# Kernel tuning notes

Measured on AMD Instinct MI355X. Metric: run time of the kernel, lower is better.

## Reference

```python
import jax, jax.numpy as jnp
import numpy as np

B, D, H, S, REP, OUT = 4096, 256, 256, 3, 10, 44


def setup_inputs():
    key = jax.random.key(0)
    ks = jax.random.split(key, 30)
    def rn(k, shape, scale=1.0):
        return jax.random.normal(k, shape, dtype=jnp.float32) * scale
    w = 0.05
    return {
        "x": rn(ks[0], (B, D)),
        "hidden0": rn(ks[1], (S, B, H)),
        "current0": rn(ks[2], (S, B, H)),
        "Wi_f": rn(ks[3], (S, H, D), w), "bi_f": rn(ks[4], (S, H), w),
        "Wi_i": rn(ks[5], (S, H, D), w), "bi_i": rn(ks[6], (S, H), w),
        "Wi_o": rn(ks[7], (S, H, D), w), "bi_o": rn(ks[8], (S, H), w),
        "Wi_c": rn(ks[9], (S, H, D), w), "bi_c": rn(ks[10], (S, H), w),
        "Wi_g": rn(ks[11], (S, S, D), w), "bi_g": rn(ks[12], (S, S), w),
        "Wh_f": rn(ks[13], (S, H, H), w), "bh_f": rn(ks[14], (S, H), w),
        "Wh_i": rn(ks[15], (S, H, H), w), "bh_i": rn(ks[16], (S, H), w),
        "Wh_o": rn(ks[17], (S, H, H), w), "bh_o": rn(ks[18], (S, H), w),
        "Wh_g": rn(ks[19], (S, S, S * H), w), "bh_g": rn(ks[20], (S, S), w),
        "Wh_c": rn(ks[21], (S, S * H, S * H), w), "bh_c": rn(ks[22], (S, S * H), w),
        "W_last": rn(ks[23], (OUT, (REP - 1) * H), w), "b_last": rn(ks[24], (OUT,), w),
    }


def _lin(x, W, b):
    return x @ W.T + b


def _gflstm(x, hidden0, current0, Wi_f, bi_f, Wi_i, bi_i, Wi_o, bi_o, Wi_c, bi_c,
            Wi_g, bi_g, Wh_f, bh_f, Wh_i, bh_i, Wh_o, bh_o, Wh_g, bh_g,
            Wh_c, bh_c, W_last, b_last):
    S_, B_, H_ = hidden0.shape
    rep = W_last.shape[1] // H_ + 1  # (rep_time-1)*H in-features of last layer
    h_prev, c_prev = hidden0, current0
    last_layer_hs = []
    for t in range(rep):  # fixed small trip-count, sequential recurrence
        # torch.cat(hidden[t], 1): layer-major concat -> [B, S*H]
        h_cat = jnp.transpose(h_prev, (1, 0, 2)).reshape(B_, S_ * H_)
        input_h = x
        h_list, c_list = [], []
        for l in range(S_):
            f = jax.nn.sigmoid(_lin(input_h, Wi_f[l], bi_f[l]) + _lin(h_prev[l], Wh_f[l], bh_f[l]))
            i = jax.nn.sigmoid(_lin(input_h, Wi_i[l], bi_i[l]) + _lin(h_prev[l], Wh_i[l], bh_i[l]))
            g = jax.nn.sigmoid(_lin(input_h, Wi_g[l], bi_g[l]) + _lin(h_cat, Wh_g[l], bh_g[l]))  # [B, S]
            aux = _lin(h_cat, Wh_c[l], bh_c[l]).reshape(B_, S_, H_)
            aux = (aux * g[:, :, None]).sum(axis=1)  # gated cross-layer weighted sum -> [B, H]
            c_t = jnp.tanh(_lin(input_h, Wi_c[l], bi_c[l]) + aux)
            c = f * c_prev[l] + i * c_t
            o = jax.nn.sigmoid(_lin(input_h, Wi_o[l], bi_o[l]) + _lin(h_prev[l], Wh_o[l], bh_o[l]))
            h = o * c
            input_h = h
            h_list.append(h)
            c_list.append(c)
        h_prev = jnp.stack(h_list)
        c_prev = jnp.stack(c_list)
        if t < rep - 1:  # output uses hidden[1..rep-1][-1]
            last_layer_hs.append(h_list[-1])
    feat = jnp.concatenate(last_layer_hs, axis=1)  # [B, (rep-1)*H]
    return jax.nn.sigmoid(_lin(feat, W_last, b_last))


def reference(x, hidden0, current0, Wi_f, bi_f, Wi_i, bi_i, Wi_o, bi_o, Wi_c, bi_c,
              Wi_g, bi_g, Wh_f, bh_f, Wh_i, bh_i, Wh_o, bh_o, Wh_g, bh_g,
              Wh_c, bh_c, W_last, b_last):
    return _gflstm(x, hidden0, current0, Wi_f, bi_f, Wi_i, bi_i, Wi_o, bi_o, Wi_c, bi_c,
                   Wi_g, bi_g, Wh_f, bh_f, Wh_i, bh_i, Wh_o, bh_o, Wh_g, bh_g,
                   Wh_c, bh_c, W_last, b_last)
```

## Files before the change

### kernel.cpp

```cpp
#include <hip/hip_runtime.h>
#include <hip/hip_bf16.h>

typedef __hip_bfloat16 bf16;
typedef __attribute__((ext_vector_type(8))) short frag8;
typedef __attribute__((ext_vector_type(4))) float f32x4;

#define BM 128
#define BN 128
#define BK 64
#define SK 72

__device__ __forceinline__ float sigm(float x) { return 1.f / (1.f + __expf(-x)); }

__device__ __forceinline__ void lds_load16(const bf16* g, short* l) {
    __builtin_amdgcn_global_load_lds(
        (const __attribute__((address_space(1))) void*)g,
        (__attribute__((address_space(3))) void*)l, 16, 0, 0);
}

__global__ __launch_bounds__(256, 2)
void gemm_bt(const bf16* __restrict__ A, int lda, long long sAz,
             const bf16* __restrict__ W, int ldw, long long sWz,
             void* __restrict__ Cv, int ldc, long long sCz, int K,
             int outmode, const float* __restrict__ bias, int nbound,
             const bf16* __restrict__ Wg, float* __restrict__ gout)
{
    __shared__ short As[BM * SK];
    __shared__ short Bs[BN * SK];
    __shared__ short Bg[16 * SK];
    const int z = blockIdx.z;
    A += (size_t)z * sAz;
    W += (size_t)z * sWz;
    const int m0 = blockIdx.y * BM;
    const int n0 = blockIdx.x * BN;
    const int tid  = threadIdx.x;
    const int lane = tid & 63;
    const int wave = tid >> 6;
    const int wm = (wave >> 1) * 64;
    const int wn = (wave & 1) * 64;
    const int q   = lane >> 4;
    const int r16 = lane & 15;
    const bool do_g = (Wg != nullptr) && (blockIdx.x == 0);

    f32x4 acc[4][4] = {};
    f32x4 accg[4] = {};

    const int trow = tid >> 3;
    const int tcol = (tid & 7) * 8;

    for (int k0 = 0; k0 < K; k0 += BK) {
        __syncthreads();
        #pragma unroll
        for (int p = 0; p < 4; ++p) {
            int rr = p * 32 + trow;
            *(uint4*)&As[rr * SK + tcol] =
                *(const uint4*)(A + (size_t)(m0 + rr) * lda + k0 + tcol);
            *(uint4*)&Bs[rr * SK + tcol] =
                *(const uint4*)(W + (size_t)(n0 + rr) * ldw + k0 + tcol);
        }
        if (do_g && tid < 128)
            *(uint4*)&Bg[(tid >> 3) * SK + tcol] =
                *(const uint4*)(Wg + (size_t)(tid >> 3) * 256 + k0 + tcol);
        __syncthreads();
        #pragma unroll
        for (int kk = 0; kk < 2; ++kk) {
            const int ko = kk * 32 + q * 8;
            frag8 af[4], bfr[4];
            #pragma unroll
            for (int i = 0; i < 4; ++i)
                af[i] = *(const frag8*)&As[(wm + i * 16 + r16) * SK + ko];
            #pragma unroll
            for (int j = 0; j < 4; ++j)
                bfr[j] = *(const frag8*)&Bs[(wn + j * 16 + r16) * SK + ko];
            #pragma unroll
            for (int i = 0; i < 4; ++i)
                #pragma unroll
                for (int j = 0; j < 4; ++j)
                    acc[i][j] = __builtin_amdgcn_mfma_f32_16x16x32_bf16(
                        af[i], bfr[j], acc[i][j], 0, 0, 0);
            if (do_g) {
                frag8 bg = *(const frag8*)&Bg[r16 * SK + ko];
                #pragma unroll
                for (int i = 0; i < 4; ++i)
                    accg[i] = __builtin_amdgcn_mfma_f32_16x16x32_bf16(
                        af[i], bg, accg[i], 0, 0, 0);
            }
        }
    }

    if (outmode == 0) {
        float* C = (float*)Cv + (size_t)z * sCz;
        #pragma unroll
        for (int i = 0; i < 4; ++i)
            #pragma unroll
            for (int rr = 0; rr < 4; ++rr) {
                int row = m0 + wm + i * 16 + q * 4 + rr;
                float* crow = C + (size_t)row * ldc + n0 + wn + r16;
                #pragma unroll
                for (int j = 0; j < 4; ++j) crow[j * 16] = acc[i][j][rr];
            }
    } else if (outmode == 1) {
        bf16* C = (bf16*)Cv + (size_t)z * sCz;
        #pragma unroll
        for (int i = 0; i < 4; ++i)
            #pragma unroll
            for (int rr = 0; rr < 4; ++rr) {
                int row = m0 + wm + i * 16 + q * 4 + rr;
                bf16* crow = C + (size_t)row * ldc + n0 + wn + r16;
                #pragma unroll
                for (int j = 0; j < 4; ++j) crow[j * 16] = __float2bfloat16(acc[i][j][rr]);
            }
    } else if (outmode == 2) {
        float* C = (float*)Cv + (size_t)z * sCz;
        #pragma unroll
        for (int i = 0; i < 4; ++i)
            #pragma unroll
            for (int rr = 0; rr < 4; ++rr) {
                int row = m0 + wm + i * 16 + q * 4 + rr;
                #pragma unroll
                for (int j = 0; j < 4; ++j) {
                    int col = n0 + wn + j * 16 + r16;
                    if (col < nbound)
                        C[(size_t)row * ldc + col] = sigm(acc[i][j][rr] + bias[col]);
                }
            }
    } else {
        float* C = (float*)Cv + (size_t)z * sCz;
        #pragma unroll
        for (int i = 0; i < 4; ++i)
            #pragma unroll
            for (int rr = 0; rr < 4; ++rr) {
                int row = m0 + wm + i * 16 + q * 4 + rr;
                #pragma unroll
                for (int j = 0; j < 4; ++j) {
                    int col = n0 + wn + j * 16 + r16;
                    if (col < nbound)
                        C[(size_t)row * ldc + col] = acc[i][j][rr];
                }
            }
    }
    if (do_g && wn == 0 && r16 < 3) {
        #pragma unroll
        for (int i = 0; i < 4; ++i)
            #pragma unroll
            for (int rr = 0; rr < 4; ++rr) {
                int row = m0 + wm + i * 16 + q * 4 + rr;
                gout[(size_t)row * 3 + r16] = accg[i][rr];
            }
    }
}

__global__ __launch_bounds__(256, 3)
void gemm_hidden(const bf16* __restrict__ hprev,
                 const bf16* __restrict__ WhFIO,
                 const bf16* __restrict__ WhCb,
                 const bf16* __restrict__ WgH,
                 const float* __restrict__ big, const float* __restrict__ bhg,
                 bf16* __restrict__ hgb,
                 bf16* __restrict__ auxb,
                 float* __restrict__ gh)
{
    __shared__ __align__(16) short As[BM * 64];
    __shared__ __align__(16) short Bs[BN * 64];
    __shared__ __align__(16) short Bg[16 * 64];

    const int zi = blockIdx.x % 6;
    const int xt = blockIdx.x / 6;
    const bool isaux = zi >= 3;
    const int l = isaux ? zi - 3 : zi;
    const bf16* A = hprev + (isaux ? 0 : l * 256);
    const int K = isaux ? 768 : 256;
    const bf16* W = isaux ? (WhCb + (size_t)l * 768 * 768) : (WhFIO + (size_t)l * 768 * 256);
    const int ldw = isaux ? 768 : 256;
    bf16* C = (isaux ? auxb : hgb) + (size_t)l * 4096 * 768;
    const bool do_g = isaux && (xt == 0);

    const int m0 = blockIdx.y * BM;
    const int n0 = xt * BN;
    const int tid  = threadIdx.x;
    const int lane = tid & 63;
    const int wave = tid >> 6;
    const int wm = (wave >> 1) * 64;
    const int wn = (wave & 1) * 64;
    const int q   = lane >> 4;
    const int r16 = lane & 15;

    f32x4 acc[4][4] = {};
    f32x4 accg[4] = {};

    const int srow = lane >> 3;
    const int scolsw = ((lane & 7) ^ srow) * 8;
    const bf16* WgL = WgH + (size_t)l * 16 * 768;

    for (int k0 = 0; k0 < K; k0 += BK) {
        __syncthreads();
        #pragma unroll
        for (int p = 0; p < 4; ++p) {
            int rbase = (wave * 4 + p) * 8;
            lds_load16(A + (size_t)(m0 + rbase + srow) * 768 + k0 + scolsw, &As[rbase * 64]);
            lds_load16(W + (size_t)(n0 + rbase + srow) * ldw + k0 + scolsw, &Bs[rbase * 64]);
        }
        if (do_g && wave < 2)
            lds_load16(WgL + (size_t)(wave * 8 + srow) * 768 + k0 + scolsw, &Bg[wave * 8 * 64]);
        __syncthreads();
        #pragma unroll
        for (int kk = 0; kk < 2; ++kk) {
            const int c = kk * 4 + q;
            frag8 af[4], bfr[4];
            #pragma unroll
            for (int i = 0; i < 4; ++i) {
                int R = wm + i * 16 + r16;
                af[i] = *(const frag8*)&As[R * 64 + ((c ^ (R & 7)) << 3)];
            }
            #pragma unroll
            for (int j = 0; j < 4; ++j) {
                int R = wn + j * 16 + r16;
                bfr[j] = *(const frag8*)&Bs[R * 64 + ((c ^ (R & 7)) << 3)];
            }
            #pragma unroll
            for (int i = 0; i < 4; ++i)
                #pragma unroll
                for (int j = 0; j < 4; ++j)
                    acc[i][j] = __builtin_amdgcn_mfma_f32_16x16x32_bf16(
                        af[i], bfr[j], acc[i][j], 0, 0, 0);
            if (do_g) {
                frag8 bg = *(const frag8*)&Bg[r16 * 64 + ((c ^ (r16 & 7)) << 3)];
                #pragma unroll
                for (int i = 0; i < 4; ++i)
                    accg[i] = __builtin_amdgcn_mfma_f32_16x16x32_bf16(
                        af[i], bg, accg[i], 0, 0, 0);
            }
        }
    }

    #pragma unroll
    for (int i = 0; i < 4; ++i)
        #pragma unroll
        for (int rr = 0; rr < 4; ++rr) {
            int row = m0 + wm + i * 16 + q * 4 + rr;
            bf16* crow = C + (size_t)row * 768 + n0 + wn + r16;
            #pragma unroll
            for (int j = 0; j < 4; ++j) crow[j * 16] = __float2bfloat16(acc[i][j][rr]);
        }
    if (do_g && wn == 0 && r16 < 3) {
        float bsum = big[l * 3 + r16] + bhg[l * 3 + r16];
        #pragma unroll
        for (int i = 0; i < 4; ++i)
            #pragma unroll
            for (int rr = 0; rr < 4; ++rr) {
                int row = m0 + wm + i * 16 + q * 4 + rr;
                gh[(size_t)row * 9 + l * 3 + r16] = accg[i][rr] + bsum;
            }
    }
}

#define GM 32
struct Stage { short As[GM * 64]; short Bs[BN * 64]; short Bg[16 * 64]; };
union SMemU { Stage s; float ct[GM * 128]; };

__global__ __launch_bounds__(256, 2)
void gemm_gates(const bf16* __restrict__ A, int lda,
                const bf16* __restrict__ Wi, const bf16* __restrict__ Wg,
                const bf16* __restrict__ hg_l,
                const bf16* __restrict__ aux_l,
                const float* __restrict__ ghc_l,
                const float* __restrict__ cprev,
                const float* __restrict__ bif, const float* __restrict__ bhf,
                const float* __restrict__ bii, const float* __restrict__ bhi,
                const float* __restrict__ bio, const float* __restrict__ bho,
                const float* __restrict__ bic, const float* __restrict__ bhc,
                bf16*  __restrict__ hnew,
                float* __restrict__ cnew,
                bf16*  __restrict__ featc)
{
    __shared__ __align__(16) SMemU sm;
    __shared__ float gsh[GM * 3];

    const int m0 = blockIdx.y * GM;
    const int n0 = blockIdx.x * BN;
    const int jbase = n0 >> 2;
    const int tid  = threadIdx.x;
    const int lane = tid & 63;
    const int wave = tid >> 6;
    const int wm = (wave >> 1) * 16;
    const int wn = (wave & 1) * 64;
    const int q   = lane >> 4;
    const int r16 = lane & 15;

    f32x4 acc[4] = {};
    f32x4 accg = {};

    const int srow = lane >> 3;
    const int scolsw = ((lane & 7) ^ srow) * 8;

    for (int k0 = 0; k0 < 256; k0 += BK) {
        __syncthreads();
        lds_load16(A + (size_t)(m0 + wave * 8 + srow) * lda + k0 + scolsw,
                   &sm.s.As[wave * 8 * 64]);
        #pragma unroll
        for (int p = 0; p < 4; ++p) {
            int rbase = (wave * 4 + p) * 8;
            lds_load16(Wi + (size_t)(n0 + rbase + srow) * 256 + k0 + scolsw, &sm.s.Bs[rbase * 64]);
        }
        if (wave < 2)
            lds_load16(Wg + (size_t)(wave * 8 + srow) * 256 + k0 + scolsw, &sm.s.Bg[wave * 8 * 64]);
        __syncthreads();
        #pragma unroll
        for (int kk = 0; kk < 2; ++kk) {
            const int c = kk * 4 + q;
            frag8 af, bfr[4], bg;
            bg = *(const frag8*)&sm.s.Bg[r16 * 64 + ((c ^ (r16 & 7)) << 3)];
            {
                int R = wm + r16;
                af = *(const frag8*)&sm.s.As[R * 64 + ((c ^ (R & 7)) << 3)];
            }
            #pragma unroll
            for (int j = 0; j < 4; ++j) {
                int R = wn + j * 16 + r16;
                bfr[j] = *(const frag8*)&sm.s.Bs[R * 64 + ((c ^ (R & 7)) << 3)];
            }
            #pragma unroll
            for (int j = 0; j < 4; ++j)
                acc[j] = __builtin_amdgcn_mfma_f32_16x16x32_bf16(af, bfr[j], acc[j], 0, 0, 0);
            accg = __builtin_amdgcn_mfma_f32_16x16x32_bf16(af, bg, accg, 0, 0, 0);
        }
    }

    __syncthreads();
    if (wn == 0 && r16 < 3) {
        #pragma unroll
        for (int rr = 0; rr < 4; ++rr) {
            int row = wm + q * 4 + rr;
            gsh[row * 3 + r16] = sigm(accg[rr] + ghc_l[(size_t)(m0 + row) * 9 + r16]);
        }
    }
    #pragma unroll
    for (int rr = 0; rr < 4; ++rr) {
        int rowl = wm + q * 4 + rr;
        #pragma unroll
        for (int jr = 0; jr < 4; ++jr) {
            int col = wn + jr * 16 + r16;
            sm.ct[rowl * 128 + ((col + 4 * rowl) & 127)] = acc[jr][rr];
        }
    }
    __syncthreads();

    const int jj = tid & 31;
    const int r0 = (tid >> 5) * 4;
    const int j  = jbase + jj;
    const float vbif = bif[j], vbhf = bhf[j];
    const float vbii = bii[j], vbhi = bhi[j];
    const float vbio = bio[j], vbho = bho[j];
    const float vbic = bic[j];
    const float vbc0 = bhc[j], vbc1 = bhc[256 + j], vbc2 = bhc[512 + j];

    #pragma unroll
    for (int ri = 0; ri < 4; ++ri) {
        int rowl = r0 + ri;
        size_t b = m0 + rowl;
        float4 pre = *(float4*)&sm.ct[rowl * 128 + ((4 * jj + 4 * rowl) & 127)];
        float g0 = gsh[rowl * 3 + 0];
        float g1 = gsh[rowl * 3 + 1];
        float g2 = gsh[rowl * 3 + 2];
        float hgf = __bfloat162float(hg_l[b * 768 + j]);
        float hgi = __bfloat162float(hg_l[b * 768 + 256 + j]);
        float hgo = __bfloat162float(hg_l[b * 768 + 512 + j]);
        float ax0 = __bfloat162float(aux_l[b * 768 + j]);
        float ax1 = __bfloat162float(aux_l[b * 768 + 256 + j]);
        float ax2 = __bfloat162float(aux_l[b * 768 + 512 + j]);
        float f  = sigm(pre.x + vbif + hgf + vbhf);
        float ii = sigm(pre.y + vbii + hgi + vbhi);
        float o  = sigm(pre.z + vbio + hgo + vbho);
        float av = g0 * (ax0 + vbc0) + g1 * (ax1 + vbc1) + g2 * (ax2 + vbc2);
        float ct = tanhf(pre.w + vbic + av);
        float c  = f * cprev[b * 256 + j] + ii * ct;
        float h  = o * c;
        cnew[b * 256 + j] = c;
        hnew[b * 768 + j] = __float2bfloat16(h);
        if (featc) featc[b * 2304 + j] = __float2bfloat16(h);
    }
}

__global__ __launch_bounds__(256)
void gates_pre(const bf16* __restrict__ ipre0i, const float* __restrict__ gin0,
               const float* __restrict__ ghc,
               const bf16* __restrict__ hg_l, const bf16* __restrict__ aux_l,
               const float* __restrict__ cprev,
               const float* __restrict__ bif, const float* __restrict__ bhf,
               const float* __restrict__ bii, const float* __restrict__ bhi,
               const float* __restrict__ bio, const float* __restrict__ bho,
               const float* __restrict__ bic, const float* __restrict__ bhc,
               bf16* __restrict__ hnew, float* __restrict__ cnew)
{
    const int j = threadIdx.x;
    const int b0 = blockIdx.x * 4;
    const float vbif = bif[j], vbhf = bhf[j];
    const float vbii = bii[j], vbhi = bhi[j];
    const float vbio = bio[j], vbho = bho[j];
    const float vbic = bic[j];
    const float vbc0 = bhc[j], vbc1 = bhc[256 + j], vbc2 = bhc[512 + j];

    #pragma unroll
    for (int r = 0; r < 4; ++r) {
        const size_t b = b0 + r;
        const bf16* ip4 = ipre0i + b * 1024 + 4 * j;
        float pf = __bfloat162float(ip4[0]);
        float pi = __bfloat162float(ip4[1]);
        float po = __bfloat162float(ip4[2]);
        float pc = __bfloat162float(ip4[3]);
        float g0 = sigm(gin0[b * 3 + 0] + ghc[b * 9 + 0]);
        float g1 = sigm(gin0[b * 3 + 1] + ghc[b * 9 + 1]);
        float g2 = sigm(gin0[b * 3 + 2] + ghc[b * 9 + 2]);
        float hgf = __bfloat162float(hg_l[b * 768 + j]);
        float hgi = __bfloat162float(hg_l[b * 768 + 256 + j]);
        float hgo = __bfloat162float(hg_l[b * 768 + 512 + j]);
        float ax0 = __bfloat162float(aux_l[b * 768 + j]);
        float ax1 = __bfloat162float(aux_l[b * 768 + 256 + j]);
        float ax2 = __bfloat162float(aux_l[b * 768 + 512 + j]);
        float f  = sigm(pf + vbif + hgf + vbhf);
        float ii = sigm(pi + vbii + hgi + vbhi);
        float o  = sigm(po + vbio + hgo + vbho);
        float av = g0 * (ax0 + vbc0) + g1 * (ax1 + vbc1) + g2 * (ax2 + vbc2);
        float ct = tanhf(pc + vbic + av);
        float c  = f * cprev[b * 256 + j] + ii * ct;
        float h  = o * c;
        cnew[b * 256 + j] = c;
        hnew[b * 768 + j] = __float2bfloat16(h);
    }
}

__global__ __launch_bounds__(256)
void final_reduce(const float* __restrict__ part, const float* __restrict__ bl,
                  float* __restrict__ out)
{
    int idx = blockIdx.x * 256 + threadIdx.x;
    if (idx >= 4096 * 44) return;
    int b = idx / 44, n = idx - b * 44;
    float s = bl[n];
    #pragma unroll
    for (int z = 0; z < 12; ++z) s += part[(size_t)z * 4096 * 64 + (size_t)b * 64 + n];
    out[idx] = sigm(s);
}

__global__ __launch_bounds__(256)
void prep_all(const float* __restrict__ Wi_f, const float* __restrict__ Wi_i,
              const float* __restrict__ Wi_o, const float* __restrict__ Wi_c,
              const float* __restrict__ Wh_f, const float* __restrict__ Wh_i,
              const float* __restrict__ Wh_o, const float* __restrict__ Wh_c,
              const float* __restrict__ Wi_g, const float* __restrict__ Wh_g,
              const float* __restrict__ W_last, const float* __restrict__ x,
              const float* __restrict__ hidden0, const float* __restrict__ current0,
              bf16* __restrict__ WiCatI, bf16* __restrict__ WhFIO,
              bf16* __restrict__ WhCb, bf16* __restrict__ Wgb,
              bf16* __restrict__ WgH, bf16* __restrict__ Wlb,
              bf16* __restrict__ xb, bf16* __restrict__ hcat, float* __restrict__ c0)
{
    int idx = blockIdx.x * 256 + threadIdx.x;
    if (idx < 786432) {
        int k = idx & 255, n = (idx >> 8) & 1023, l = idx >> 18;
        int j = n >> 2, g = n & 3;
        const float* src = (g == 0) ? Wi_f : (g == 1) ? Wi_i : (g == 2) ? Wi_o : Wi_c;
        WiCatI[idx] = __float2bfloat16(src[l * 65536 + j * 256 + k]);
        return;
    }
    idx -= 786432;
    if (idx < 589824) {
        int k = idx & 255, n = (idx >> 8) % 768, l = idx / 196608;
        const float* src = (n < 256) ? Wh_f : (n < 512) ? Wh_i : Wh_o;
        WhFIO[idx] = __float2bfloat16(src[l * 65536 + (n & 255) * 256 + k]);
        return;
    }
    idx -= 589824;
    if (idx < 1769472) {
        WhCb[idx] = __float2bfloat16(Wh_c[idx]);
        return;
    }
    idx -= 1769472;
    if (idx < 12288) {
        int k = idx & 255, r = (idx >> 8) & 15, l = idx >> 12;
        Wgb[idx] = (r < 3) ? __float2bfloat16(Wi_g[l * 768 + r * 256 + k])
                           : __float2bfloat16(0.f);
        return;
    }
    idx -= 12288;
    if (idx < 36864) {
        int k = idx % 768, r = (idx / 768) & 15, l = idx / (16 * 768);
        WgH[idx] = (r < 3) ? __float2bfloat16(Wh_g[(l * 3 + r) * 768 + k])
                           : __float2bfloat16(0.f);
        return;
    }
    idx -= 36864;
    if (idx < 294912) {
        int k = idx % 2304, n = idx / 2304;
        Wlb[idx] = (n < 44) ? __float2bfloat16(W_last[n * 2304 + k])
                            : __float2bfloat16(0.f);
        return;
    }
    idx -= 294912;
    if (idx < 1048576) {
        xb[idx] = __float2bfloat16(x[idx]);
        return;
    }
    idx -= 1048576;
    if (idx < 3145728) {
        int j = idx & 255, b = (idx >> 8) & 4095, l = idx >> 20;
        hcat[(size_t)b * 768 + l * 256 + j] = __float2bfloat16(hidden0[idx]);
        c0[idx] = current0[idx];
    }
}

extern "C" void kernel_launch(void* const* d_in, const int* in_sizes, int n_in,
                              void* d_out, int out_size, void* d_ws, size_t ws_size,
                              hipStream_t stream)
{
    (void)in_sizes; (void)n_in; (void)out_size; (void)ws_size;
    const float* x        = (const float*)d_in[0];
    const float* hidden0  = (const float*)d_in[1];
    const float* current0 = (const float*)d_in[2];
    const float* Wi_f = (const float*)d_in[3];  const float* bi_f = (const float*)d_in[4];
    const float* Wi_i = (const float*)d_in[5];  const float* bi_i = (const float*)d_in[6];
    const float* Wi_o = (const float*)d_in[7];  const float* bi_o = (const float*)d_in[8];
    const float* Wi_c = (const float*)d_in[9];  const float* bi_c = (const float*)d_in[10];
    const float* Wi_g = (const float*)d_in[11]; const float* bi_g = (const float*)d_in[12];
    const float* Wh_f = (const float*)d_in[13]; const float* bh_f = (const float*)d_in[14];
    const float* Wh_i = (const float*)d_in[15]; const float* bh_i = (const float*)d_in[16];
    const float* Wh_o = (const float*)d_in[17]; const float* bh_o = (const float*)d_in[18];
    const float* Wh_g = (const float*)d_in[19]; const float* bh_g = (const float*)d_in[20];
    const float* Wh_c = (const float*)d_in[21]; const float* bh_c = (const float*)d_in[22];
    const float* W_last = (const float*)d_in[23]; const float* b_last = (const float*)d_in[24];

    char* p = (char*)d_ws;
    bf16* WiCatI = (bf16*)p; p += (size_t)3 * 1024 * 256 * 2;
    bf16* WhFIO  = (bf16*)p; p += (size_t)3 * 768 * 256 * 2;
    bf16* WhCb   = (bf16*)p; p += (size_t)3 * 768 * 768 * 2;
    bf16* Wgb    = (bf16*)p; p += (size_t)3 * 16 * 256 * 2;
    bf16* WgH    = (bf16*)p; p += (size_t)3 * 16 * 768 * 2;
    bf16* Wlb    = (bf16*)p; p += (size_t)128 * 2304 * 2;
    bf16* xb     = (bf16*)p; p += (size_t)4096 * 256 * 2;
    bf16* ipre0i = (bf16*)p; p += (size_t)4096 * 1024 * 2;
    float* gin0  = (float*)p; p += (size_t)4096 * 3 * 4;
    bf16* hb0    = (bf16*)p; p += (size_t)4096 * 768 * 2;
    bf16* hb1    = (bf16*)p; p += (size_t)4096 * 768 * 2;
    float* cb0   = (float*)p; p += (size_t)3 * 4096 * 256 * 4;
    float* cb1   = (float*)p; p += (size_t)3 * 4096 * 256 * 4;
    bf16* hgb    = (bf16*)p; p += (size_t)3 * 4096 * 768 * 2;
    bf16* auxb   = (bf16*)p; p += (size_t)3 * 4096 * 768 * 2;
    float* gh    = (float*)p; p += (size_t)4096 * 9 * 4;
    bf16* feat   = (bf16*)p; p += (size_t)4096 * 2304 * 2;
    float* partf = (float*)p; p += (size_t)12 * 4096 * 64 * 4;

    prep_all<<<30017, 256, 0, stream>>>(
        Wi_f, Wi_i, Wi_o, Wi_c, Wh_f, Wh_i, Wh_o, Wh_c, Wi_g, Wh_g, W_last, x,
        hidden0, current0,
        WiCatI, WhFIO, WhCb, Wgb, WgH, Wlb, xb, hb0, cb0);

    gemm_bt<<<dim3(8, 32, 1), 256, 0, stream>>>(xb, 256, 0, WiCatI, 256, 0,
                                                ipre0i, 1024, 0, 256, 1, nullptr, 0,
                                                Wgb, gin0);

    for (int t = 0; t < 10; ++t) {
        bf16* hprev = (t & 1) ? hb1 : hb0;
        bf16* hnew  = (t & 1) ? hb0 : hb1;
        float* cprev = (t & 1) ? cb1 : cb0;
        float* cnew  = (t & 1) ? cb0 : cb1;

        gemm_hidden<<<dim3(36, 32), 256, 0, stream>>>(
            hprev, WhFIO, WhCb, WgH, bi_g, bh_g, hgb, auxb, gh);

        gates_pre<<<1024, 256, 0, stream>>>(
            ipre0i, gin0, gh,
            hgb, auxb, cprev,
            bi_f, bh_f, bi_i, bh_i, bi_o, bh_o, bi_c, bh_c,
            hnew, cnew);

        for (int l = 1; l < 3; ++l) {
            gemm_gates<<<dim3(8, 128), 256, 0, stream>>>(
                (const bf16*)(hnew + (l - 1) * 256), 768,
                WiCatI + (size_t)l * 1024 * 256,
                Wgb + (size_t)l * 16 * 256,
                hgb + (size_t)l * 4096 * 768,
                auxb + (size_t)l * 4096 * 768,
                gh + l * 3,
                cprev + (size_t)l * 4096 * 256,
                bi_f + l * 256, bh_f + l * 256,
                bi_i + l * 256, bh_i + l * 256,
                bi_o + l * 256, bh_o + l * 256,
                bi_c + l * 256, bh_c + l * 768,
                hnew + l * 256,
                cnew + (size_t)l * 4096 * 256,
                (l == 2 && t < 9) ? (feat + (size_t)t * 256) : (bf16*)nullptr);
        }
    }

    gemm_bt<<<dim3(1, 32, 12), 256, 0, stream>>>(
        feat, 2304, 192, Wlb, 2304, 192,
        partf, 64, (long long)4096 * 64, 192, 3, nullptr, 64,
        nullptr, nullptr);
    final_reduce<<<704, 256, 0, stream>>>(partf, b_last, (float*)d_out);
}
```

Baseline: 782.9 us.

## Use direct global-to-LDS loads with XOR swizzle and 64-row tiles in bt GEMM

Replaces the register-staged, padded LDS tile loads in the standalone bt GEMM with global_load_lds direct-to-LDS transfers. Bank conflicts are now avoided by an XOR swizzle on the 16-byte chunk index rather than by row padding. The M tile is halved to 64 rows, which doubles the grid for the input-projection and final-layer GEMMs, and the unused output modes are dropped. This kernel only runs outside the recurrent loop, so it touches a small share of the total time. The smaller tile also lowers reuse of the W tile.

```diff
diff --git a/kernel.cpp b/kernel.cpp
--- a/kernel.cpp
+++ b/kernel.cpp
@@ -8,7 +8,6 @@
 #define BM 128
 #define BN 128
 #define BK 64
-#define SK 72
 
 __device__ __forceinline__ float sigm(float x) { return 1.f / (1.f + __expf(-x)); }
 
@@ -19,90 +18,84 @@
 }
 
 __global__ __launch_bounds__(256, 2)
-void gemm_bt(const bf16* __restrict__ A, int lda, long long sAz,
-             const bf16* __restrict__ W, int ldw, long long sWz,
-             void* __restrict__ Cv, int ldc, long long sCz, int K,
-             int outmode, const float* __restrict__ bias, int nbound,
-             const bf16* __restrict__ Wg, float* __restrict__ gout)
-{
-    __shared__ short As[BM * SK];
-    __shared__ short Bs[BN * SK];
-    __shared__ short Bg[16 * SK];
+void gemm_bt64(const bf16* __restrict__ A, int lda, long long sAz,
+               const bf16* __restrict__ W, int ldw, long long sWz,
+               void* __restrict__ Cv, int ldc, long long sCz, int K,
+               int outmode, int nbound,
+               const bf16* __restrict__ Wg, float* __restrict__ gout)
+{
+    __shared__ __align__(16) short As[64 * 64];
+    __shared__ __align__(16) short Bs[BN * 64];
+    __shared__ __align__(16) short Bg[16 * 64];
     const int z = blockIdx.z;
     A += (size_t)z * sAz;
     W += (size_t)z * sWz;
-    const int m0 = blockIdx.y * BM;
+    const int m0 = blockIdx.y * 64;
     const int n0 = blockIdx.x * BN;
     const int tid  = threadIdx.x;
     const int lane = tid & 63;
     const int wave = tid >> 6;
-    const int wm = (wave >> 1) * 64;
+    const int wm = (wave >> 1) * 32;
     const int wn = (wave & 1) * 64;
     const int q   = lane >> 4;
     const int r16 = lane & 15;
     const bool do_g = (Wg != nullptr) && (blockIdx.x == 0);
 
-    f32x4 acc[4][4] = {};
-    f32x4 accg[4] = {};
-
-    const int trow = tid >> 3;
-    const int tcol = (tid & 7) * 8;
+    f32x4 acc[2][4] = {};
+    f32x4 accg[2] = {};
+
+    const int srow = lane >> 3;
+    const int scolsw = ((lane & 7) ^ srow) * 8;
 
     for (int k0 = 0; k0 < K; k0 += BK) {
         __syncthreads();
         #pragma unroll
+        for (int p = 0; p < 2; ++p) {
+            int rbase = (wave * 2 + p) * 8;
+            lds_load16(A + (size_t)(m0 + rbase + srow) * lda + k0 + scolsw, &As[rbase * 64]);
+        }
+        #pragma unroll
         for (int p = 0; p < 4; ++p) {
-            int rr = p * 32 + trow;
-            *(uint4*)&As[rr * SK + tcol] =
-                *(const uint4*)(A + (size_t)(m0 + rr) * lda + k0 + tcol);
-            *(uint4*)&Bs[rr * SK + tcol] =
-                *(const uint4*)(W + (size_t)(n0 + rr) * ldw + k0 + tcol);
-        }
-        if (do_g && tid < 128)
-            *(uint4*)&Bg[(tid >> 3) * SK + tcol] =
-                *(const uint4*)(Wg + (size_t)(tid >> 3) * 256 + k0 + tcol);
+            int rbase = (wave * 4 + p) * 8;
+            lds_load16(W + (size_t)(n0 + rbase + srow) * ldw + k0 + scolsw, &Bs[rbase * 64]);
+        }
+        if (do_g && wave < 2)
+            lds_load16(Wg + (size_t)(wave * 8 + srow) * lda + k0 + scolsw, &Bg[wave * 8 * 64]);
         __syncthreads();
         #pragma unroll
         for (int kk = 0; kk < 2; ++kk) {
-            const int ko = kk * 32 + q * 8;
-            frag8 af[4], bfr[4];
-            #pragma unroll
-            for (int i = 0; i < 4; ++i)
-                af[i] = *(const frag8*)&As[(wm + i * 16 + r16) * SK + ko];
-            #pragma unroll
-            for (int j = 0; j < 4; ++j)
-                bfr[j] = *(const frag8*)&Bs[(wn + j * 16 + r16) * SK + ko];
-            #pragma unroll
-            for (int i = 0; i < 4; ++i)
+            const int c = kk * 4 + q;
+            frag8 af[2], bfr[4];
+            #pragma unroll
+            for (int i = 0; i < 2; ++i) {
+                int R = wm + i * 16 + r16;
+                af[i] = *(const frag8*)&As[R * 64 + ((c ^ (R & 7)) << 3)];
+            }
+            #pragma unroll
+            for (int j = 0; j < 4; ++j) {
+                int R = wn + j * 16 + r16;
+                bfr[j] = *(const frag8*)&Bs[R * 64 + ((c ^ (R & 7)) << 3)];
+            }
+            #pragma unroll
+            for (int i = 0; i < 2; ++i)
                 #pragma unroll
                 for (int j = 0; j < 4; ++j)
                     acc[i][j] = __builtin_amdgcn_mfma_f32_16x16x32_bf16(
                         af[i], bfr[j], acc[i][j], 0, 0, 0);
             if (do_g) {
-                frag8 bg = *(const frag8*)&Bg[r16 * SK + ko];
+                frag8 bg = *(const frag8*)&Bg[r16 * 64 + ((c ^ (r16 & 7)) << 3)];
                 #pragma unroll
-                for (int i = 0; i < 4; ++i)
+                for (int i = 0; i < 2; ++i)
                     accg[i] = __builtin_amdgcn_mfma_f32_16x16x32_bf16(
                         af[i], bg, accg[i], 0, 0, 0);
             }
         }
     }
 
-    if (outmode == 0) {
-        float* C = (float*)Cv + (size_t)z * sCz;
-        #pragma unroll
-        for (int i = 0; i < 4; ++i)
-            #pragma unroll
-            for (int rr = 0; rr < 4; ++rr) {
-                int row = m0 + wm + i * 16 + q * 4 + rr;
-                float* crow = C + (size_t)row * ldc + n0 + wn + r16;
-                #pragma unroll
-                for (int j = 0; j < 4; ++j) crow[j * 16] = acc[i][j][rr];
-            }
-    } else if (outmode == 1) {
+    if (outmode == 1) {
         bf16* C = (bf16*)Cv + (size_t)z * sCz;
         #pragma unroll
-        for (int i = 0; i < 4; ++i)
+        for (int i = 0; i < 2; ++i)
             #pragma unroll
             for (int rr = 0; rr < 4; ++rr) {
                 int row = m0 + wm + i * 16 + q * 4 + rr;
@@ -110,24 +103,10 @@
                 #pragma unroll
                 for (int j = 0; j < 4; ++j) crow[j * 16] = __float2bfloat16(acc[i][j][rr]);
             }
-    } else if (outmode == 2) {
-        float* C = (float*)Cv + (size_t)z * sCz;
-        #pragma unroll
-        for (int i = 0; i < 4; ++i)
-            #pragma unroll
-            for (int rr = 0; rr < 4; ++rr) {
-                int row = m0 + wm + i * 16 + q * 4 + rr;
-                #pragma unroll
-                for (int j = 0; j < 4; ++j) {
-                    int col = n0 + wn + j * 16 + r16;
-                    if (col < nbound)
-                        C[(size_t)row * ldc + col] = sigm(acc[i][j][rr] + bias[col]);
-                }
-            }
     } else {
         float* C = (float*)Cv + (size_t)z * sCz;
         #pragma unroll
-        for (int i = 0; i < 4; ++i)
+        for (int i = 0; i < 2; ++i)
             #pragma unroll
             for (int rr = 0; rr < 4; ++rr) {
                 int row = m0 + wm + i * 16 + q * 4 + rr;
@@ -141,7 +120,7 @@
     }
     if (do_g && wn == 0 && r16 < 3) {
         #pragma unroll
-        for (int i = 0; i < 4; ++i)
+        for (int i = 0; i < 2; ++i)
             #pragma unroll
             for (int rr = 0; rr < 4; ++rr) {
                 int row = m0 + wm + i * 16 + q * 4 + rr;
@@ -554,9 +533,9 @@
         hidden0, current0,
         WiCatI, WhFIO, WhCb, Wgb, WgH, Wlb, xb, hb0, cb0);
 
-    gemm_bt<<<dim3(8, 32, 1), 256, 0, stream>>>(xb, 256, 0, WiCatI, 256, 0,
-                                                ipre0i, 1024, 0, 256, 1, nullptr, 0,
-                                                Wgb, gin0);
+    gemm_bt64<<<dim3(8, 64, 1), 256, 0, stream>>>(xb, 256, 0, WiCatI, 256, 0,
+                                                  ipre0i, 1024, 0, 256, 1, 0,
+                                                  Wgb, gin0);
 
     for (int t = 0; t < 10; ++t) {
         bf16* hprev = (t & 1) ? hb1 : hb0;
@@ -592,9 +571,9 @@
         }
     }
 
-    gemm_bt<<<dim3(1, 32, 12), 256, 0, stream>>>(
+    gemm_bt64<<<dim3(1, 64, 12), 256, 0, stream>>>(
         feat, 2304, 192, Wlb, 2304, 192,
-        partf, 64, (long long)4096 * 64, 192, 3, nullptr, 64,
+        partf, 64, (long long)4096 * 64, 192, 3, 64,
         nullptr, nullptr);
     final_reduce<<<704, 256, 0, stream>>>(partf, b_last, (float*)d_out);
 }
```

Measured after the change: 778.6 us. Within noise of the previous version (-0.6%).
